# Kernel tuning notes

Measured on AMD Instinct MI355X. Metric: run time of the kernel, lower is better.

The kernel has to match this reference:

```python
import jax, jax.numpy as jnp
import numpy as np

N_NODES = 100000


def gcn_conv(x, src, dst, W, b, n_nodes):
    # PyG GCNConv: add self-loops, sym-normalize, transform then aggregate.
    loop = jnp.arange(n_nodes, dtype=src.dtype)
    s = jnp.concatenate([src, loop])
    d = jnp.concatenate([dst, loop])
    ones = jnp.ones(s.shape[0], dtype=x.dtype)
    deg = jax.ops.segment_sum(ones, d, num_segments=n_nodes)
    dinv = jnp.where(deg > 0, jax.lax.rsqrt(deg), 0.0)
    norm = dinv[s] * dinv[d]  # [E+N]
    h = x @ W                 # [N, out]
    msg = h[s] * norm[:, None]
    out = jax.ops.segment_sum(msg, d, num_segments=n_nodes)
    return out + b


def setup_inputs() -> dict:
    key = jax.random.key(0)
    ks = jax.random.split(key, 10)
    n, f = N_NODES, 128
    x = jax.random.normal(ks[0], (n, f), dtype=jnp.float32)
    edge_index = jax.random.randint(ks[1], (2, 1600000), 0, n, dtype=jnp.int64)

    def glorot(k, fin, fout):
        lim = float(np.sqrt(6.0 / (fin + fout)))
        return jax.random.uniform(k, (fin, fout), jnp.float32, -lim, lim)

    return {
        "x": x,
        "edge_index": edge_index,
        "W1": glorot(ks[2], f, 128), "b1": jnp.zeros((128,), jnp.float32),
        "W2": glorot(ks[3], 128, 64), "b2": jnp.zeros((64,), jnp.float32),
        "W3": glorot(ks[4], 64, 32), "b3": jnp.zeros((32,), jnp.float32),
        "Wc": glorot(ks[5], 64, 1), "bc": jnp.zeros((1,), jnp.float32),
    }


def reference(x, edge_index, W1, b1, W2, b2, W3, b3, Wc, bc):
    n = x.shape[0]
    src, dst = edge_index[0], edge_index[1]
    h = jax.nn.relu(gcn_conv(x, src, dst, W1, b1, n))   # dropout: eval mode
    h = jax.nn.relu(gcn_conv(h, src, dst, W2, b2, n))
    h = jax.nn.relu(gcn_conv(h, src, dst, W3, b3, n))
    edge_feat = jnp.concatenate([h[src], h[dst]], axis=1)  # [E, 64]
    return edge_feat @ Wc + bc
```

## Files before the change

kernel.cpp:

```cpp
#include <hip/hip_runtime.h>


typedef unsigned short u16;
typedef short bfrag __attribute__((ext_vector_type(8)));
typedef float ffrag __attribute__((ext_vector_type(4)));

#define BSHIFT 8
#define MAXB   512
#define BIN_CHUNK 4096
#define BCAP   4608

static __device__ __forceinline__ float4 f4add(float4 a, float4 b) {
    return make_float4(a.x + b.x, a.y + b.y, a.z + b.z, a.w + b.w);
}

static __device__ __forceinline__ u16 f2bf(float f) {
    unsigned u = __float_as_uint(f);
    u = (u + 0x7FFFu + ((u >> 16) & 1u)) >> 16;
    return (u16)u;
}

static __device__ __forceinline__ void bfacc2(float& a0, float& a1, unsigned u) {
    a0 += __uint_as_float(u << 16);
    a1 += __uint_as_float(u & 0xFFFF0000u);
}


__global__ __launch_bounds__(256) void init_cursors(int* __restrict__ bcur, int B) {
    int i = blockIdx.x * 256 + threadIdx.x;
    if (i < B) bcur[i] = i * BCAP;
}

__global__ __launch_bounds__(256) void bin_edges(const int* __restrict__ src,
                                                 const int* __restrict__ dst,
                                                 int* __restrict__ bcur,
                                                 unsigned* __restrict__ pairs,
                                                 int E, int B) {
    __shared__ int h[MAXB];
    __shared__ int base[MAXB];
    const int t = threadIdx.x;
    const int e0 = blockIdx.x * BIN_CHUNK;
    const int eEnd = min(e0 + BIN_CHUNK, E);
    for (int i = t; i < B; i += 256) h[i] = 0;
    __syncthreads();
    for (int e = e0 + t; e < eEnd; e += 256)
        atomicAdd(&h[dst[e] >> BSHIFT], 1);
    __syncthreads();
    for (int i = t; i < B; i += 256) {
        int c = h[i];
        base[i] = c ? atomicAdd(&bcur[i], c) : 0;
        h[i] = 0;
    }
    __syncthreads();
    for (int e = e0 + t; e < eEnd; e += 256) {
        int d = dst[e];
        int b = d >> BSHIFT;
        int pos = base[b] + atomicAdd(&h[b], 1);
        pairs[pos] = ((unsigned)(d & 255) << 24) | (unsigned)src[e];
    }
}

__global__ __launch_bounds__(256) void build_csr(const unsigned* __restrict__ pairs,
                                                 const int* __restrict__ bcur,
                                                 int* __restrict__ rowp,
                                                 int* __restrict__ rowe,
                                                 float* __restrict__ dinv,
                                                 int* __restrict__ ssrc, int N) {
    __shared__ int s[256];
    __shared__ int cur[256];
    const int t = threadIdx.x;
    const int b = blockIdx.x;
    const int eBeg = b * BCAP, eEnd = bcur[b];
    const int nodeBase = b << BSHIFT;
    s[t] = 0;
    __syncthreads();
    for (int e = eBeg + t; e < eEnd; e += 256)
        atomicAdd(&s[pairs[e] >> 24], 1);
    __syncthreads();
    const int v = s[t];
    #pragma unroll
    for (int off = 1; off < 256; off <<= 1) {
        int add = (t >= off) ? s[t - off] : 0;
        __syncthreads();
        s[t] += add;
        __syncthreads();
    }
    const int rp = eBeg + s[t] - v;
    const int node = nodeBase + t;
    if (node < N) {
        rowp[node] = rp;
        rowe[node] = rp + v;
        dinv[node] = rsqrtf((float)(v + 1));
    }
    cur[t] = rp;
    __syncthreads();
    for (int e = eBeg + t; e < eEnd; e += 256) {
        unsigned p = pairs[e];
        int pos = atomicAdd(&cur[p >> 24], 1);
        ssrc[pos] = (int)(p & 0xFFFFFFu);
    }
}

__global__ __launch_bounds__(256) void prep_w(const float* __restrict__ W,
                                              u16* __restrict__ Wt, int K, int Nc) {
    int idx = blockIdx.x * 256 + threadIdx.x;
    if (idx < K * Nc) {
        int n = idx / K, k = idx - n * K;
        Wt[idx] = f2bf(W[(size_t)k * Nc + n]);
    }
}

template <int FIN, int FOUT, bool AF32, int MINW>
__global__ __launch_bounds__(256, MINW)
void gemm_mfma(const void* __restrict__ Xv, const u16* __restrict__ Wt,
               const float* __restrict__ dinv, u16* __restrict__ G, int N) {
    constexpr int NT = FOUT / 16;
    constexpr int KK = FIN / 32;
    constexpr int CB = FIN / 8;
    constexpr int ITER = (64 * CB) / 256;
    __shared__ __align__(16) u16 xs[64 * FIN];
    __shared__ float ldv[64];

    const int t = threadIdx.x;
    const int wave = t >> 6;
    const int lane = t & 63;
    const int l15 = lane & 15;
    const int quad = lane >> 4;
    const int r0 = blockIdx.x * 64;

    bfrag Bf[NT][KK];
    #pragma unroll
    for (int nt = 0; nt < NT; nt++)
        #pragma unroll
        for (int kk = 0; kk < KK; kk++)
            Bf[nt][kk] = *reinterpret_cast<const bfrag*>(
                &Wt[(size_t)(nt * 16 + l15) * FIN + kk * 32 + quad * 8]);

    if (t < 64) ldv[t] = (r0 + t < N) ? dinv[r0 + t] : 0.f;

    #pragma unroll
    for (int i = 0; i < ITER; i++) {
        int v = t + 256 * i;
        int row = v / CB;
        int cb = v - row * CB;
        uint4 pack = make_uint4(0, 0, 0, 0);
        if (r0 + row < N) {
            if (AF32) {
                const float* X = (const float*)Xv;
                const float4* p = reinterpret_cast<const float4*>(
                    &X[(size_t)(r0 + row) * FIN + cb * 8]);
                float4 lo = p[0], hi = p[1];
                pack.x = f2bf(lo.x) | ((unsigned)f2bf(lo.y) << 16);
                pack.y = f2bf(lo.z) | ((unsigned)f2bf(lo.w) << 16);
                pack.z = f2bf(hi.x) | ((unsigned)f2bf(hi.y) << 16);
                pack.w = f2bf(hi.z) | ((unsigned)f2bf(hi.w) << 16);
            } else {
                const u16* X = (const u16*)Xv;
                pack = *reinterpret_cast<const uint4*>(
                    &X[(size_t)(r0 + row) * FIN + cb * 8]);
            }
        }
        int cbs = cb ^ (row & 7);
        *reinterpret_cast<uint4*>(&xs[row * FIN + cbs * 8]) = pack;
    }
    __syncthreads();

    ffrag acc[NT];
    #pragma unroll
    for (int nt = 0; nt < NT; nt++) {
        acc[nt][0] = 0.f; acc[nt][1] = 0.f; acc[nt][2] = 0.f; acc[nt][3] = 0.f;
    }

    const int arow = wave * 16 + l15;
    #pragma unroll
    for (int kk = 0; kk < KK; kk++) {
        int cb = (kk * 4 + quad) ^ (l15 & 7);
        bfrag a = *reinterpret_cast<const bfrag*>(&xs[arow * FIN + cb * 8]);
        #pragma unroll
        for (int nt = 0; nt < NT; nt++)
            acc[nt] = __builtin_amdgcn_mfma_f32_16x16x32_bf16(a, Bf[nt][kk], acc[nt], 0, 0, 0);
    }

    #pragma unroll
    for (int nt = 0; nt < NT; nt++)
        #pragma unroll
        for (int r = 0; r < 4; r++) {
            int rl = wave * 16 + quad * 4 + r;
            int grow = r0 + rl;
            if (grow < N)
                G[(size_t)grow * FOUT + nt * 16 + l15] = f2bf(acc[nt][r] * ldv[rl]);
        }
}

template <int F, bool OUT_BF16>
__global__ __launch_bounds__(256) void aggregate_bf16(const u16* __restrict__ G,
                                                      const int* __restrict__ rowp,
                                                      const int* __restrict__ rowe,
                                                      const int* __restrict__ ssrc,
                                                      const float* __restrict__ dinv,
                                                      const float* __restrict__ bias,
                                                      void* __restrict__ Hout, int N) {
    constexpr int L = F / 8;
    constexpr int NPB = 256 / L;
    const int t = threadIdx.x;
    const int lj = t % L;
    const int d = blockIdx.x * NPB + t / L;
    if (d >= N) return;

    const uint4* G4 = reinterpret_cast<const uint4*>(G);
    float a[8];
    #pragma unroll
    for (int i = 0; i < 8; i++) a[i] = 0.f;
    {
        uint4 u = G4[(size_t)d * L + lj];
        bfacc2(a[0], a[1], u.x); bfacc2(a[2], a[3], u.y);
        bfacc2(a[4], a[5], u.z); bfacc2(a[6], a[7], u.w);
    }
    int e = rowp[d];
    const int end = rowe[d];
    for (; e + 8 <= end; e += 8) {
        int si[8];
        #pragma unroll
        for (int k = 0; k < 8; k++) si[k] = ssrc[e + k];
        uint4 u[8];
        #pragma unroll
        for (int k = 0; k < 8; k++) u[k] = G4[(size_t)si[k] * L + lj];
        #pragma unroll
        for (int k = 0; k < 8; k++) {
            bfacc2(a[0], a[1], u[k].x); bfacc2(a[2], a[3], u[k].y);
            bfacc2(a[4], a[5], u[k].z); bfacc2(a[6], a[7], u[k].w);
        }
    }
    for (; e < end; e++) {
        uint4 u = G4[(size_t)ssrc[e] * L + lj];
        bfacc2(a[0], a[1], u.x); bfacc2(a[2], a[3], u.y);
        bfacc2(a[4], a[5], u.z); bfacc2(a[6], a[7], u.w);
    }
    const float dv = dinv[d];
    const float4 b0 = reinterpret_cast<const float4*>(bias)[lj * 2];
    const float4 b1 = reinterpret_cast<const float4*>(bias)[lj * 2 + 1];
    float h[8];
    h[0] = fmaxf(a[0] * dv + b0.x, 0.f);
    h[1] = fmaxf(a[1] * dv + b0.y, 0.f);
    h[2] = fmaxf(a[2] * dv + b0.z, 0.f);
    h[3] = fmaxf(a[3] * dv + b0.w, 0.f);
    h[4] = fmaxf(a[4] * dv + b1.x, 0.f);
    h[5] = fmaxf(a[5] * dv + b1.y, 0.f);
    h[6] = fmaxf(a[6] * dv + b1.z, 0.f);
    h[7] = fmaxf(a[7] * dv + b1.w, 0.f);
    if (OUT_BF16) {
        uint4 pk;
        pk.x = f2bf(h[0]) | ((unsigned)f2bf(h[1]) << 16);
        pk.y = f2bf(h[2]) | ((unsigned)f2bf(h[3]) << 16);
        pk.z = f2bf(h[4]) | ((unsigned)f2bf(h[5]) << 16);
        pk.w = f2bf(h[6]) | ((unsigned)f2bf(h[7]) << 16);
        reinterpret_cast<uint4*>(Hout)[(size_t)d * L + lj] = pk;
    } else {
        float4* H4 = reinterpret_cast<float4*>(Hout);
        H4[(size_t)d * (F / 4) + lj * 2]     = make_float4(h[0], h[1], h[2], h[3]);
        H4[(size_t)d * (F / 4) + lj * 2 + 1] = make_float4(h[4], h[5], h[6], h[7]);
    }
}

__global__ __launch_bounds__(256) void aggregate_l3s(const float* __restrict__ G,
                                                     const int* __restrict__ rowp,
                                                     const int* __restrict__ rowe,
                                                     const int* __restrict__ ssrc,
                                                     const float* __restrict__ dinv,
                                                     const float* __restrict__ bias,
                                                     const float* __restrict__ Wc,
                                                     float* __restrict__ aArr,
                                                     float* __restrict__ bArr, int N) {
    constexpr int L = 8;
    const int t = threadIdx.x;
    const int lj = t % L;
    const int d = blockIdx.x * 32 + t / L;
    if (d >= N) return;

    const float4* G4 = reinterpret_cast<const float4*>(G);
    float4 acc = G4[(size_t)d * L + lj];
    int e = rowp[d];
    const int end = rowe[d];
    for (; e + 8 <= end; e += 8) {
        int si[8];
        #pragma unroll
        for (int k = 0; k < 8; k++) si[k] = ssrc[e + k];
        float4 v[8];
        #pragma unroll
        for (int k = 0; k < 8; k++) v[k] = G4[(size_t)si[k] * L + lj];
        #pragma unroll
        for (int k = 0; k < 8; k++) acc = f4add(acc, v[k]);
    }
    for (; e < end; e++)
        acc = f4add(acc, G4[(size_t)ssrc[e] * L + lj]);
    const float dv = dinv[d];
    const float4 b4 = reinterpret_cast<const float4*>(bias)[lj];
    float4 h;
    h.x = fmaxf(acc.x * dv + b4.x, 0.f);
    h.y = fmaxf(acc.y * dv + b4.y, 0.f);
    h.z = fmaxf(acc.z * dv + b4.z, 0.f);
    h.w = fmaxf(acc.w * dv + b4.w, 0.f);
    const float4 wa = reinterpret_cast<const float4*>(Wc)[lj];
    const float4 wb = reinterpret_cast<const float4*>(Wc + 32)[lj];
    float p = h.x * wa.x + h.y * wa.y + h.z * wa.z + h.w * wa.w;
    float q = h.x * wb.x + h.y * wb.y + h.z * wb.z + h.w * wb.w;
    p += __shfl_xor(p, 1); q += __shfl_xor(q, 1);
    p += __shfl_xor(p, 2); q += __shfl_xor(q, 2);
    p += __shfl_xor(p, 4); q += __shfl_xor(q, 4);
    if (lj == 0) {
        aArr[d] = p;
        bArr[d] = q;
    }
}

template <int FIN, int FOUT, int JG, int JT, int ROWS>
__global__ __launch_bounds__(256) void gemm_dinv(const float* __restrict__ X,
                                                 const float* __restrict__ W,
                                                 const float* __restrict__ dinv,
                                                 float* __restrict__ G, int N) {
    constexpr int GROUPS = 256 / JG;
    constexpr int RPT = ROWS / GROUPS;
    __shared__ float xs[ROWS * FIN];
    const int t = threadIdx.x;
    const int r0 = blockIdx.x * ROWS;

    constexpr int NV = ROWS * FIN / 4;
    const float4* X4 = reinterpret_cast<const float4*>(X + (size_t)r0 * FIN);
    float4* xs4 = reinterpret_cast<float4*>(xs);
    #pragma unroll
    for (int v = t; v < NV; v += 256) {
        int row = v / (FIN / 4);
        float4 val = make_float4(0.f, 0.f, 0.f, 0.f);
        if (r0 + row < N) val = X4[v];
        xs4[v] = val;
    }
    __syncthreads();

    const int jg = t % JG;
    const int grp = t / JG;
    float acc[RPT][JT];
    #pragma unroll
    for (int r = 0; r < RPT; r++)
        #pragma unroll
        for (int jj = 0; jj < JT; jj++) acc[r][jj] = 0.f;

    #pragma unroll 2
    for (int k0 = 0; k0 < FIN; k0 += 8) {
        float wr[8][JT];
        #pragma unroll
        for (int q = 0; q < 8; q++)
            #pragma unroll
            for (int jj = 0; jj < JT; jj++)
                wr[q][jj] = W[(k0 + q) * FOUT + jg + jj * JG];
        #pragma unroll
        for (int r = 0; r < RPT; r++) {
            const int lr = grp * RPT + r;
            float xv[8];
            #pragma unroll
            for (int q = 0; q < 8; q++) xv[q] = xs[lr * FIN + k0 + q];
            #pragma unroll
            for (int q = 0; q < 8; q++)
                #pragma unroll
                for (int jj = 0; jj < JT; jj++)
                    acc[r][jj] += xv[q] * wr[q][jj];
        }
    }

    #pragma unroll
    for (int r = 0; r < RPT; r++) {
        const int gr = r0 + grp * RPT + r;
        if (gr < N) {
            const float dv = dinv[gr];
            #pragma unroll
            for (int jj = 0; jj < JT; jj++)
                G[(size_t)gr * FOUT + jg + jj * JG] = acc[r][jj] * dv;
        }
    }
}


__global__ __launch_bounds__(256) void edge_out(const int* __restrict__ src,
                                                const int* __restrict__ dst,
                                                const float* __restrict__ aArr,
                                                const float* __restrict__ bArr,
                                                const float* __restrict__ bc,
                                                float* __restrict__ out, int E) {
    int e = blockIdx.x * 256 + threadIdx.x;
    if (e < E) out[e] = aArr[src[e]] + bArr[dst[e]] + bc[0];
}

extern "C" void kernel_launch(void* const* d_in, const int* in_sizes, int n_in,
                              void* d_out, int out_size, void* d_ws, size_t ws_size,
                              hipStream_t stream) {
    const float* x  = (const float*)d_in[0];
    const int*   ei = (const int*)d_in[1];
    const float* W1 = (const float*)d_in[2];
    const float* b1 = (const float*)d_in[3];
    const float* W2 = (const float*)d_in[4];
    const float* b2 = (const float*)d_in[5];
    const float* W3 = (const float*)d_in[6];
    const float* b3 = (const float*)d_in[7];
    const float* Wc = (const float*)d_in[8];
    const float* bc = (const float*)d_in[9];
    float* out = (float*)d_out;

    const int N = in_sizes[0] / 128;
    const int E = in_sizes[1] / 2;
    const int B = (N + 255) >> BSHIFT;
    const int* src = ei;
    const int* dst = ei + E;

    size_t off = 0;
    auto alloc = [&](size_t bytes) -> void* {
        size_t o = (off + 255) & ~(size_t)255;
        off = o + bytes;
        return (void*)((char*)d_ws + o);
    };
    float* dinv = (float*)alloc((size_t)N * 4);
    int*   rowp = (int*)alloc((size_t)N * 4);
    int*   rowe = (int*)alloc((size_t)N * 4);
    int*   bcur = (int*)alloc((size_t)(B + 1) * 4);
    int*   ssrc = (int*)alloc((size_t)B * BCAP * 4);
    u16*   w1t  = (u16*)alloc(128 * 128 * 2);
    u16*   w2t  = (u16*)alloc(128 * 64 * 2);
    u16*   g16  = (u16*)alloc((size_t)N * 128 * 2);
    u16*   h1b  = (u16*)alloc((size_t)N * 128 * 2);
    float* h2f  = (float*)alloc((size_t)N * 64 * 4);
    float* aArr = (float*)alloc((size_t)N * 4);
    float* bArr = (float*)alloc((size_t)N * 4);
    (void)ws_size; (void)n_in; (void)out_size;

    unsigned* pairs = (unsigned*)h1b;
    float* g3f = (float*)g16;

    const int gE = (E + 255) / 256;
    const int gR = (N + 63) / 64;

    init_cursors<<<(B + 255) / 256, 256, 0, stream>>>(bcur, B);
    bin_edges<<<(E + BIN_CHUNK - 1) / BIN_CHUNK, 256, 0, stream>>>(src, dst, bcur, pairs, E, B);
    build_csr<<<B, 256, 0, stream>>>(pairs, bcur, rowp, rowe, dinv, ssrc, N);

    prep_w<<<64, 256, 0, stream>>>(W1, w1t, 128, 128);
    prep_w<<<32, 256, 0, stream>>>(W2, w2t, 128, 64);

    gemm_mfma<128, 128, true, 2><<<gR, 256, 0, stream>>>(x, w1t, dinv, g16, N);
    aggregate_bf16<128, true><<<(N + 15) / 16, 256, 0, stream>>>(g16, rowp, rowe, ssrc, dinv, b1, h1b, N);
    gemm_mfma<128, 64, false, 4><<<gR, 256, 0, stream>>>(h1b, w2t, dinv, g16, N);
    aggregate_bf16<64, false><<<(N + 31) / 32, 256, 0, stream>>>(g16, rowp, rowe, ssrc, dinv, b2, h2f, N);
    gemm_dinv<64, 32, 32, 1, 32><<<(N + 31) / 32, 256, 0, stream>>>(h2f, W3, dinv, g3f, N);
    aggregate_l3s<<<(N + 31) / 32, 256, 0, stream>>>(g3f, rowp, rowe, ssrc, dinv, b3, Wc, aArr, bArr, N);

    edge_out<<<gE, 256, 0, stream>>>(src, dst, aArr, bArr, bc, out, E);
}
```

Measured before the change: 362.5 us.

## Merge weight prep kernels, reduce gather unroll, interleave per-node edge scores

Merges the two weight transpose/convert launches into one kernel. Cuts the gather unroll in the bf16 and layer-3 aggregation loops from 8 to 4 edges per iteration, lowering register pressure but also reducing the number of loads in flight. Packs the per-node source and destination scores into one float2 array, so edge_out reads 8-byte records instead of two separate float arrays.

```diff
diff --git a/kernel.cpp b/kernel.cpp
--- a/kernel.cpp
+++ b/kernel.cpp
@@ -101,12 +101,18 @@
     }
 }
 
-__global__ __launch_bounds__(256) void prep_w(const float* __restrict__ W,
-                                              u16* __restrict__ Wt, int K, int Nc) {
+__global__ __launch_bounds__(256) void prep_w2(const float* __restrict__ W1,
+                                               u16* __restrict__ W1t,
+                                               const float* __restrict__ W2,
+                                               u16* __restrict__ W2t) {
     int idx = blockIdx.x * 256 + threadIdx.x;
-    if (idx < K * Nc) {
-        int n = idx / K, k = idx - n * K;
-        Wt[idx] = f2bf(W[(size_t)k * Nc + n]);
+    if (idx < 128 * 128) {
+        int n = idx >> 7, k = idx & 127;
+        W1t[idx] = f2bf(W1[k * 128 + n]);
+    } else if (idx < 128 * 128 + 64 * 128) {
+        int j = idx - 128 * 128;
+        int n = j >> 7, k = j & 127;
+        W2t[j] = f2bf(W2[k * 64 + n]);
     }
 }
 
@@ -218,18 +224,20 @@
     }
     int e = rowp[d];
     const int end = rowe[d];
-    for (; e + 8 <= end; e += 8) {
-        int si[8];
-        #pragma unroll
-        for (int k = 0; k < 8; k++) si[k] = ssrc[e + k];
-        uint4 u[8];
-        #pragma unroll
-        for (int k = 0; k < 8; k++) u[k] = G4[(size_t)si[k] * L + lj];
-        #pragma unroll
-        for (int k = 0; k < 8; k++) {
-            bfacc2(a[0], a[1], u[k].x); bfacc2(a[2], a[3], u[k].y);
-            bfacc2(a[4], a[5], u[k].z); bfacc2(a[6], a[7], u[k].w);
-        }
+    for (; e + 4 <= end; e += 4) {
+        int s0 = ssrc[e], s1 = ssrc[e + 1], s2 = ssrc[e + 2], s3 = ssrc[e + 3];
+        uint4 u0 = G4[(size_t)s0 * L + lj];
+        uint4 u1 = G4[(size_t)s1 * L + lj];
+        uint4 u2 = G4[(size_t)s2 * L + lj];
+        uint4 u3 = G4[(size_t)s3 * L + lj];
+        bfacc2(a[0], a[1], u0.x); bfacc2(a[2], a[3], u0.y);
+        bfacc2(a[4], a[5], u0.z); bfacc2(a[6], a[7], u0.w);
+        bfacc2(a[0], a[1], u1.x); bfacc2(a[2], a[3], u1.y);
+        bfacc2(a[4], a[5], u1.z); bfacc2(a[6], a[7], u1.w);
+        bfacc2(a[0], a[1], u2.x); bfacc2(a[2], a[3], u2.y);
+        bfacc2(a[4], a[5], u2.z); bfacc2(a[6], a[7], u2.w);
+        bfacc2(a[0], a[1], u3.x); bfacc2(a[2], a[3], u3.y);
+        bfacc2(a[4], a[5], u3.z); bfacc2(a[6], a[7], u3.w);
     }
     for (; e < end; e++) {
         uint4 u = G4[(size_t)ssrc[e] * L + lj];
@@ -269,8 +277,7 @@
                                                      const float* __restrict__ dinv,
                                                      const float* __restrict__ bias,
                                                      const float* __restrict__ Wc,
-                                                     float* __restrict__ aArr,
-                                                     float* __restrict__ bArr, int N) {
+                                                     float2* __restrict__ ab, int N) {
     constexpr int L = 8;
     const int t = threadIdx.x;
     const int lj = t % L;
@@ -281,15 +288,13 @@
     float4 acc = G4[(size_t)d * L + lj];
     int e = rowp[d];
     const int end = rowe[d];
-    for (; e + 8 <= end; e += 8) {
-        int si[8];
-        #pragma unroll
-        for (int k = 0; k < 8; k++) si[k] = ssrc[e + k];
-        float4 v[8];
-        #pragma unroll
-        for (int k = 0; k < 8; k++) v[k] = G4[(size_t)si[k] * L + lj];
-        #pragma unroll
-        for (int k = 0; k < 8; k++) acc = f4add(acc, v[k]);
+    for (; e + 4 <= end; e += 4) {
+        int s0 = ssrc[e], s1 = ssrc[e + 1], s2 = ssrc[e + 2], s3 = ssrc[e + 3];
+        float4 v0 = G4[(size_t)s0 * L + lj];
+        float4 v1 = G4[(size_t)s1 * L + lj];
+        float4 v2 = G4[(size_t)s2 * L + lj];
+        float4 v3 = G4[(size_t)s3 * L + lj];
+        acc = f4add(acc, f4add(f4add(v0, v1), f4add(v2, v3)));
     }
     for (; e < end; e++)
         acc = f4add(acc, G4[(size_t)ssrc[e] * L + lj]);
@@ -307,10 +312,7 @@
     p += __shfl_xor(p, 1); q += __shfl_xor(q, 1);
     p += __shfl_xor(p, 2); q += __shfl_xor(q, 2);
     p += __shfl_xor(p, 4); q += __shfl_xor(q, 4);
-    if (lj == 0) {
-        aArr[d] = p;
-        bArr[d] = q;
-    }
+    if (lj == 0) ab[d] = make_float2(p, q);
 }
 
 template <int FIN, int FOUT, int JG, int JT, int ROWS>
@@ -381,12 +383,11 @@
 
 __global__ __launch_bounds__(256) void edge_out(const int* __restrict__ src,
                                                 const int* __restrict__ dst,
-                                                const float* __restrict__ aArr,
-                                                const float* __restrict__ bArr,
+                                                const float2* __restrict__ ab,
                                                 const float* __restrict__ bc,
                                                 float* __restrict__ out, int E) {
     int e = blockIdx.x * 256 + threadIdx.x;
-    if (e < E) out[e] = aArr[src[e]] + bArr[dst[e]] + bc[0];
+    if (e < E) out[e] = ab[src[e]].x + ab[dst[e]].y + bc[0];
 }
 
 extern "C" void kernel_launch(void* const* d_in, const int* in_sizes, int n_in,
@@ -426,8 +427,7 @@
     u16*   g16  = (u16*)alloc((size_t)N * 128 * 2);
     u16*   h1b  = (u16*)alloc((size_t)N * 128 * 2);
     float* h2f  = (float*)alloc((size_t)N * 64 * 4);
-    float* aArr = (float*)alloc((size_t)N * 4);
-    float* bArr = (float*)alloc((size_t)N * 4);
+    float2* ab  = (float2*)alloc((size_t)N * 8);
     (void)ws_size; (void)n_in; (void)out_size;
 
     unsigned* pairs = (unsigned*)h1b;
@@ -440,15 +440,14 @@
     bin_edges<<<(E + BIN_CHUNK - 1) / BIN_CHUNK, 256, 0, stream>>>(src, dst, bcur, pairs, E, B);
     build_csr<<<B, 256, 0, stream>>>(pairs, bcur, rowp, rowe, dinv, ssrc, N);
 
-    prep_w<<<64, 256, 0, stream>>>(W1, w1t, 128, 128);
-    prep_w<<<32, 256, 0, stream>>>(W2, w2t, 128, 64);
+    prep_w2<<<96, 256, 0, stream>>>(W1, w1t, W2, w2t);
 
     gemm_mfma<128, 128, true, 2><<<gR, 256, 0, stream>>>(x, w1t, dinv, g16, N);
     aggregate_bf16<128, true><<<(N + 15) / 16, 256, 0, stream>>>(g16, rowp, rowe, ssrc, dinv, b1, h1b, N);
     gemm_mfma<128, 64, false, 4><<<gR, 256, 0, stream>>>(h1b, w2t, dinv, g16, N);
     aggregate_bf16<64, false><<<(N + 31) / 32, 256, 0, stream>>>(g16, rowp, rowe, ssrc, dinv, b2, h2f, N);
     gemm_dinv<64, 32, 32, 1, 32><<<(N + 31) / 32, 256, 0, stream>>>(h2f, W3, dinv, g3f, N);
-    aggregate_l3s<<<(N + 31) / 32, 256, 0, stream>>>(g3f, rowp, rowe, ssrc, dinv, b3, Wc, aArr, bArr, N);
-
-    edge_out<<<gE, 256, 0, stream>>>(src, dst, aArr, bArr, bc, out, E);
-}
+    aggregate_l3s<<<(N + 31) / 32, 256, 0, stream>>>(g3f, rowp, rowe, ssrc, dinv, b3, Wc, ab, N);
+
+    edge_out<<<gE, 256, 0, stream>>>(src, dst, ab, bc, out, E);
+}
```

Result: faster. 349.0 us (-3.7%).
